# Performance work log

Hardware: AMD Instinct MI355X
Metric: run time of the kernel (lower is better)

The kernel has to match this reference:

```python
import jax, jax.numpy as jnp
import numpy as np

S, B = 64, 256
CH_IN, CH_OUT, AUX, HID = 128, 128, 3, 32
EPS = 1e-5


def _ln(h, g, b):
    mu = jnp.mean(h, axis=-1, keepdims=True)
    var = jnp.mean(jnp.square(h - mu), axis=-1, keepdims=True)
    return (h - mu) * jax.lax.rsqrt(var + EPS) * g + b


def _hyper_mlp(z, W1, b1, g1, be1, W2, b2, g2, be2, W3, b3):
    # Linear -> LN -> ReLU -> Linear -> LN -> ReLU -> Linear (droprate=0)
    h = jax.nn.relu(_ln(jnp.einsum('sba,ha->sbh', z, W1) + b1, g1, be1))
    h = jax.nn.relu(_ln(jnp.einsum('sbh,kh->sbk', h, W2) + b2, g2, be2))
    return jnp.einsum('sbh,oh->sbo', h, W3) + b3


def setup_inputs() -> dict:
    key = jax.random.key(0)
    ks = jax.random.split(key, 24)
    f = lambda k, shp: (jax.random.normal(k, shp, dtype=jnp.float32) * 0.05)
    inp = {
        'x': jax.random.normal(ks[0], (S, B, CH_IN), dtype=jnp.float32),
        'z': jax.random.normal(ks[1], (S, B, AUX), dtype=jnp.float32),
        # weight-branch hypernet params
        'wW1': f(ks[2], (HID, AUX)), 'wb1': jnp.zeros((HID,), jnp.float32),
        'wg1': jnp.ones((HID,), jnp.float32), 'wbe1': jnp.zeros((HID,), jnp.float32),
        'wW2': f(ks[3], (HID, HID)), 'wb2': jnp.zeros((HID,), jnp.float32),
        'wg2': jnp.ones((HID,), jnp.float32), 'wbe2': jnp.zeros((HID,), jnp.float32),
        'wW3': f(ks[4], (CH_OUT * CH_IN, HID)), 'wb3': jnp.zeros((CH_OUT * CH_IN,), jnp.float32),
        # bias-branch hypernet params
        'bW1': f(ks[5], (HID, AUX)), 'bb1': jnp.zeros((HID,), jnp.float32),
        'bg1': jnp.ones((HID,), jnp.float32), 'bbe1': jnp.zeros((HID,), jnp.float32),
        'bW2': f(ks[6], (HID, HID)), 'bb2': jnp.zeros((HID,), jnp.float32),
        'bg2': jnp.ones((HID,), jnp.float32), 'bbe2': jnp.zeros((HID,), jnp.float32),
        'bW3': f(ks[7], (CH_OUT, HID)), 'bb3': jnp.zeros((CH_OUT,), jnp.float32),
    }
    return inp


def reference(x, z,
              wW1, wb1, wg1, wbe1, wW2, wb2, wg2, wbe2, wW3, wb3,
              bW1, bb1, bg1, bbe1, bW2, bb2, bg2, bbe2, bW3, bb3):
    # per-token weight: [S,B,ch_out*ch_in] -> [S,B,ch_out,ch_in]
    weight = _hyper_mlp(z, wW1, wb1, wg1, wbe1, wW2, wb2, wg2, wbe2, wW3, wb3)
    weight = weight.reshape(S, B, CH_OUT, CH_IN)
    bias = _hyper_mlp(z, bW1, bb1, bg1, bbe1, bW2, bb2, bg2, bbe2, bW3, bb3)
    # batched mat-vec: out[s,b,o] = sum_i weight[s,b,o,i] * x[s,b,i] + bias
    out = jnp.einsum('sboi,sbi->sbo', weight, x) + bias
    return out
```

## Files before the change

### kernel.cpp

```cpp
#include <hip/hip_runtime.h>
#include <hip/hip_fp16.h>
#include <stdint.h>

#define KR      4288
#define LN_EPS  1e-5f

typedef _Float16 f16;
typedef __attribute__((ext_vector_type(2))) _Float16 h2v;
typedef __attribute__((ext_vector_type(4))) _Float16 h4v;
typedef __attribute__((ext_vector_type(8))) _Float16 h8v;
typedef __attribute__((ext_vector_type(4))) float    f32x4;

union H2U { uint32_t u; h2v h; };
union H8U { uint32_t u[4]; h8v v; };

__global__ __launch_bounds__(256) void prep_w3(
    const float* __restrict__ wW3, const float* __restrict__ wb3,
    const float* __restrict__ bW3, f16* __restrict__ w3h)
{
  const int cid = blockIdx.x * 256 + threadIdx.x;
  const int o   = blockIdx.y;
  if (cid >= KR / 8) return;
  const int k0    = cid * 8;
  const int slice = k0 >> 5;
  const int h0    = k0 & 31;
  float v[8];
  if (slice < 133) {
    const float* src;
    if      (slice < 128) src = wW3 + ((size_t)o * 128 + slice) * 32 + h0;
    else if (slice < 132) src = wb3 + (size_t)o * 128 + (slice - 128) * 32 + h0;
    else                  src = bW3 + (size_t)o * 32 + h0;
    float4 a = *(const float4*)src;
    float4 b = *(const float4*)(src + 4);
    v[0]=a.x; v[1]=a.y; v[2]=a.z; v[3]=a.w; v[4]=b.x; v[5]=b.y; v[6]=b.z; v[7]=b.w;
  } else {
#pragma unroll
    for (int j = 0; j < 8; ++j) v[j] = 0.f;
  }
  h8v pk;
#pragma unroll
  for (int j = 0; j < 8; ++j) pk[j] = (f16)v[j];
  *(h8v*)(w3h + (size_t)o * KR + k0) = pk;
}

__global__ __launch_bounds__(256) void fused_kernel(
    const float* __restrict__ x, const float* __restrict__ z,
    const float* __restrict__ wW1, const float* __restrict__ wb1,
    const float* __restrict__ wg1, const float* __restrict__ wbe1,
    const float* __restrict__ wW2, const float* __restrict__ wb2,
    const float* __restrict__ wg2, const float* __restrict__ wbe2,
    const float* __restrict__ bW1, const float* __restrict__ bb1,
    const float* __restrict__ bg1, const float* __restrict__ bbe1,
    const float* __restrict__ bW2, const float* __restrict__ bb2,
    const float* __restrict__ bg2, const float* __restrict__ bbe2,
    const float* __restrict__ bb3,
    const f16* __restrict__ w3h, float* __restrict__ out)
{
  __shared__ __align__(16) f16 xs[64][136];
  __shared__ __align__(16) f16 h2w_s[64][40];
  __shared__ __align__(16) f16 h2b_s[64][40];

  const int tid  = threadIdx.x;
  const int lane = tid & 63;
  const int wid  = tid >> 6;
  const int lm   = lane & 15, hc = lane >> 4, hbase = hc * 8;
  const int tile = blockIdx.x >> 1;
  const int kh   = blockIdx.x & 1;
  const int t0   = tile * 64;
  const int o0   = wid * 32;
  const int ks0    = kh * 34;
  const int n_iter = kh ? 33 : 34;

  float bbv[2];
#pragma unroll
  for (int n = 0; n < 2; ++n) bbv[n] = bb3[o0 + n * 16 + lm] * (float)kh;

  {
    const int r = tid >> 2, q = tid & 3;
    const float* src = x + (size_t)(t0 + r) * 128 + q * 32;
#pragma unroll
    for (int u = 0; u < 8; ++u) {
      float4 v = *(const float4*)(src + u * 4);
      h4v p; p[0] = (f16)v.x; p[1] = (f16)v.y; p[2] = (f16)v.z; p[3] = (f16)v.w;
      *(h4v*)&xs[r][q * 32 + u * 4] = p;
    }
  }

  if (tid < 128) {
    const int br  = tid >> 6;
    const int row = tid & 63;
    const int tok = t0 + row;
    const float* W1  = br ? bW1  : wW1;  const float* b1  = br ? bb1  : wb1;
    const float* g1  = br ? bg1  : wg1;  const float* be1 = br ? bbe1 : wbe1;
    const float* W2  = br ? bW2  : wW2;  const float* b2  = br ? bb2  : wb2;
    const float* g2  = br ? bg2  : wg2;  const float* be2 = br ? bbe2 : wbe2;

    const float z0 = z[tok * 3 + 0], z1 = z[tok * 3 + 1], z2 = z[tok * 3 + 2];

    float h1[32];
    float s = 0.f, s2 = 0.f;
#pragma unroll
    for (int j = 0; j < 32; ++j) {
      float v = W1[j * 3] * z0 + W1[j * 3 + 1] * z1 + W1[j * 3 + 2] * z2 + b1[j];
      h1[j] = v; s += v; s2 += v * v;
    }
    float mu  = s * (1.f / 32.f);
    float var = fmaxf(s2 * (1.f / 32.f) - mu * mu, 0.f);
    float rr  = rsqrtf(var + LN_EPS);
#pragma unroll
    for (int j = 0; j < 32; ++j)
      h1[j] = fmaxf((h1[j] - mu) * rr * g1[j] + be1[j], 0.f);

    float h2a[32];
    s = 0.f; s2 = 0.f;
#pragma unroll
    for (int j = 0; j < 32; ++j) {
      float acc = b2[j];
#pragma unroll
      for (int kk = 0; kk < 8; ++kk) {
        float4 w = *(const float4*)&W2[j * 32 + kk * 4];
        acc += w.x * h1[kk * 4] + w.y * h1[kk * 4 + 1]
             + w.z * h1[kk * 4 + 2] + w.w * h1[kk * 4 + 3];
      }
      h2a[j] = acc; s += acc; s2 += acc * acc;
    }
    mu  = s * (1.f / 32.f);
    var = fmaxf(s2 * (1.f / 32.f) - mu * mu, 0.f);
    rr  = rsqrtf(var + LN_EPS);
    f16* dst = br ? &h2b_s[row][0] : &h2w_s[row][0];
#pragma unroll
    for (int j4 = 0; j4 < 8; ++j4) {
      h4v w;
      w[0] = (f16)fmaxf((h2a[j4*4+0] - mu) * rr * g2[j4*4+0] + be2[j4*4+0], 0.f);
      w[1] = (f16)fmaxf((h2a[j4*4+1] - mu) * rr * g2[j4*4+1] + be2[j4*4+1], 0.f);
      w[2] = (f16)fmaxf((h2a[j4*4+2] - mu) * rr * g2[j4*4+2] + be2[j4*4+2], 0.f);
      w[3] = (f16)fmaxf((h2a[j4*4+3] - mu) * rr * g2[j4*4+3] + be2[j4*4+3], 0.f);
      *(h4v*)&dst[j4 * 4] = w;
    }
  }

  __syncthreads();

  uint32_t h2p[4][4];
#pragma unroll
  for (int m = 0; m < 4; ++m) {
    H8U c; c.v = *(const h8v*)&h2w_s[m * 16 + lm][hbase];
#pragma unroll
    for (int q = 0; q < 4; ++q) h2p[m][q] = c.u[q];
  }

  const f16* bp00 = w3h + (size_t)(o0 + lm)      * KR + (ks0 * 2    ) * 32 + hbase;
  const f16* bp01 = w3h + (size_t)(o0 + 16 + lm) * KR + (ks0 * 2    ) * 32 + hbase;
  const f16* bp10 = w3h + (size_t)(o0 + lm)      * KR + (ks0 * 2 + 1) * 32 + hbase;
  const f16* bp11 = w3h + (size_t)(o0 + 16 + lm) * KR + (ks0 * 2 + 1) * 32 + hbase;

#define LOADSET(S) do { \
    S[0][0] = *(const h8v*)bp00; bp00 += 64; \
    S[0][1] = *(const h8v*)bp01; bp01 += 64; \
    S[1][0] = *(const h8v*)bp10; bp10 += 64; \
    S[1][1] = *(const h8v*)bp11; bp11 += 64; } while (0)

  f32x4 acc[4][2];
#pragma unroll
  for (int m = 0; m < 4; ++m)
#pragma unroll
    for (int n = 0; n < 2; ++n) acc[m][n] = (f32x4){0.f, 0.f, 0.f, 0.f};

  auto STEP = [&](h8v (&bs)[2][2], int ks) {
    const int ksg = ks0 + ks;
    h8v af0[4], af1[4];
    if (ksg < 64) {
#pragma unroll
      for (int m = 0; m < 4; ++m) {
        const uint32_t xp = *(const uint32_t*)&xs[m * 16 + lm][2 * ksg];
        H2U x0, x1;
        x0.u = (xp & 0xffffu) | (xp << 16);
        x1.u = (xp >> 16) | (xp & 0xffff0000u);
        H8U r0, r1;
#pragma unroll
        for (int q = 0; q < 4; ++q) {
          H2U hq; hq.u = h2p[m][q];
          H2U p0; p0.h = x0.h * hq.h; r0.u[q] = p0.u;
          H2U p1; p1.h = x1.h * hq.h; r1.u[q] = p1.u;
        }
        af0[m] = r0.v; af1[m] = r1.v;
      }
    } else if (ksg < 66) {
      const int s = (ksg - 64) * 2;
#pragma unroll
      for (int m = 0; m < 4; ++m) {
        af0[m] = *(const h8v*)&xs[m * 16 + lm][s * 32 + hbase];
        af1[m] = *(const h8v*)&xs[m * 16 + lm][(s + 1) * 32 + hbase];
      }
    } else {
#pragma unroll
      for (int m = 0; m < 4; ++m) {
        af0[m] = *(const h8v*)&h2b_s[m * 16 + lm][hbase];
        af1[m] = af0[m];
      }
    }
#pragma unroll
    for (int n = 0; n < 2; ++n)
#pragma unroll
      for (int m = 0; m < 4; ++m)
        acc[m][n] = __builtin_amdgcn_mfma_f32_16x16x32_f16(af0[m], bs[0][n], acc[m][n], 0, 0, 0);
#pragma unroll
    for (int n = 0; n < 2; ++n)
#pragma unroll
      for (int m = 0; m < 4; ++m)
        acc[m][n] = __builtin_amdgcn_mfma_f32_16x16x32_f16(af1[m], bs[1][n], acc[m][n], 0, 0, 0);
  };

  h8v bA[2][2], bB[2][2];
  LOADSET(bA);
  LOADSET(bB);

  int ks = 0;
#pragma unroll 1
  while (ks + 2 <= n_iter) {
    STEP(bA, ks);
    if (ks + 2 < n_iter) LOADSET(bA);
    STEP(bB, ks + 1);
    if (ks + 3 < n_iter) LOADSET(bB);
    ks += 2;
  }
  if (ks < n_iter) STEP(bA, ks);

#pragma unroll
  for (int m = 0; m < 4; ++m) {
#pragma unroll
    for (int n = 0; n < 2; ++n) {
      const int gc = o0 + n * 16 + lm;
#pragma unroll
      for (int r_ = 0; r_ < 4; ++r_) {
        const int row = t0 + m * 16 + hc * 4 + r_;
        atomicAdd(&out[(size_t)row * 128 + gc], acc[m][n][r_] + bbv[n]);
      }
    }
  }
#undef LOADSET
}

extern "C" void kernel_launch(void* const* d_in, const int* in_sizes, int n_in,
                              void* d_out, int out_size, void* d_ws, size_t ws_size,
                              hipStream_t stream)
{
  const float* x    = (const float*)d_in[0];
  const float* z    = (const float*)d_in[1];
  const float* wW1  = (const float*)d_in[2];
  const float* wb1  = (const float*)d_in[3];
  const float* wg1  = (const float*)d_in[4];
  const float* wbe1 = (const float*)d_in[5];
  const float* wW2  = (const float*)d_in[6];
  const float* wb2  = (const float*)d_in[7];
  const float* wg2  = (const float*)d_in[8];
  const float* wbe2 = (const float*)d_in[9];
  const float* wW3  = (const float*)d_in[10];
  const float* wb3  = (const float*)d_in[11];
  const float* bW1  = (const float*)d_in[12];
  const float* bb1  = (const float*)d_in[13];
  const float* bg1  = (const float*)d_in[14];
  const float* bbe1 = (const float*)d_in[15];
  const float* bW2  = (const float*)d_in[16];
  const float* bb2  = (const float*)d_in[17];
  const float* bg2  = (const float*)d_in[18];
  const float* bbe2 = (const float*)d_in[19];
  const float* bW3  = (const float*)d_in[20];
  const float* bb3  = (const float*)d_in[21];

  f16*   w3h  = (f16*)d_ws;
  float* outf = (float*)d_out;

  hipMemsetAsync(d_out, 0, (size_t)16384 * 128 * sizeof(float), stream);
  hipLaunchKernelGGL(prep_w3, dim3(3, 128), dim3(256), 0, stream,
                     wW3, wb3, bW3, w3h);
  hipLaunchKernelGGL(fused_kernel, dim3(512), dim3(256), 0, stream,
                     x, z,
                     wW1, wb1, wg1, wbe1, wW2, wb2, wg2, wbe2,
                     bW1, bb1, bg1, bbe1, bW2, bb2, bg2, bbe2,
                     bb3, w3h, outf);
}
```

Before: 63.39 us.

## Split hypernet MLP into separate kernel and quad-split GEMM K dimension

```diff
diff --git a/kernel.cpp b/kernel.cpp
--- a/kernel.cpp
+++ b/kernel.cpp
@@ -2,7 +2,8 @@
 #include <hip/hip_fp16.h>
 #include <stdint.h>
 
-#define KR      4288
+#define T_DIM   16384
+#define NKS     67
 #define LN_EPS  1e-5f
 
 typedef _Float16 f16;
@@ -16,14 +17,21 @@
 
 __global__ __launch_bounds__(256) void prep_w3(
     const float* __restrict__ wW3, const float* __restrict__ wb3,
-    const float* __restrict__ bW3, f16* __restrict__ w3h)
+    const float* __restrict__ bW3, f16* __restrict__ w3p)
 {
-  const int cid = blockIdx.x * 256 + threadIdx.x;
-  const int o   = blockIdx.y;
-  if (cid >= KR / 8) return;
-  const int k0    = cid * 8;
-  const int slice = k0 >> 5;
-  const int h0    = k0 & 31;
+  const int idx  = blockIdx.x * 256 + threadIdx.x;
+  const int lane = idx & 63;
+  int rest = idx >> 6;
+  const int n  = rest & 1;  rest >>= 1;
+  const int i2 = rest & 1;  rest >>= 1;
+  const int ks = rest % 67;
+  const int os = rest / 67;
+  if (os >= 4) return;
+
+  const int o     = os * 32 + n * 16 + (lane & 15);
+  const int slice = ks * 2 + i2;
+  const int h0    = (lane >> 4) * 8;
+
   float v[8];
   if (slice < 133) {
     const float* src;
@@ -40,10 +48,10 @@
   h8v pk;
 #pragma unroll
   for (int j = 0; j < 8; ++j) pk[j] = (f16)v[j];
-  *(h8v*)(w3h + (size_t)o * KR + k0) = pk;
+  *(h8v*)(w3p + ((size_t)(os * 67 + ks) * 2048 + i2 * 1024 + n * 512 + lane * 8)) = pk;
 }
 
-__global__ __launch_bounds__(256) void fused_kernel(
+__global__ __launch_bounds__(256) void hyper_kernel(
     const float* __restrict__ x, const float* __restrict__ z,
     const float* __restrict__ wW1, const float* __restrict__ wb1,
     const float* __restrict__ wg1, const float* __restrict__ wbe1,
@@ -53,112 +61,128 @@
     const float* __restrict__ bg1, const float* __restrict__ bbe1,
     const float* __restrict__ bW2, const float* __restrict__ bb2,
     const float* __restrict__ bg2, const float* __restrict__ bbe2,
-    const float* __restrict__ bb3,
-    const f16* __restrict__ w3h, float* __restrict__ out)
+    f16* __restrict__ xf, f16* __restrict__ h2w, f16* __restrict__ h2b)
+{
+  const int tid = threadIdx.x;
+  const int bid = blockIdx.x;
+
+  {
+    const size_t base = (size_t)bid * 16384;
+#pragma unroll
+    for (int u = 0; u < 16; ++u) {
+      const size_t off = base + u * 1024 + tid * 4;
+      float4 a = *(const float4*)(x + off);
+      h4v p; p[0] = (f16)a.x; p[1] = (f16)a.y; p[2] = (f16)a.z; p[3] = (f16)a.w;
+      *(h4v*)(xf + off) = p;
+    }
+  }
+
+  const int br  = bid >> 6;
+  const int tok = (bid & 63) * 256 + tid;
+  const float* W1  = br ? bW1  : wW1;  const float* b1  = br ? bb1  : wb1;
+  const float* g1  = br ? bg1  : wg1;  const float* be1 = br ? bbe1 : wbe1;
+  const float* W2  = br ? bW2  : wW2;  const float* b2  = br ? bb2  : wb2;
+  const float* g2  = br ? bg2  : wg2;  const float* be2 = br ? bbe2 : wbe2;
+  f16* dst = (br ? h2b : h2w) + (size_t)tok * 32;
+
+  const float z0 = z[tok * 3 + 0], z1 = z[tok * 3 + 1], z2 = z[tok * 3 + 2];
+
+  float h1[32];
+  float s = 0.f, s2 = 0.f;
+#pragma unroll
+  for (int j = 0; j < 32; ++j) {
+    float v = W1[j * 3] * z0 + W1[j * 3 + 1] * z1 + W1[j * 3 + 2] * z2 + b1[j];
+    h1[j] = v; s += v; s2 += v * v;
+  }
+  float mu  = s * (1.f / 32.f);
+  float var = fmaxf(s2 * (1.f / 32.f) - mu * mu, 0.f);
+  float rr  = rsqrtf(var + LN_EPS);
+#pragma unroll
+  for (int j = 0; j < 32; ++j)
+    h1[j] = fmaxf((h1[j] - mu) * rr * g1[j] + be1[j], 0.f);
+
+  float h2a[32];
+  s = 0.f; s2 = 0.f;
+#pragma unroll
+  for (int j = 0; j < 32; ++j) {
+    float acc = b2[j];
+#pragma unroll
+    for (int kk = 0; kk < 8; ++kk) {
+      float4 w = *(const float4*)&W2[j * 32 + kk * 4];
+      acc += w.x * h1[kk * 4] + w.y * h1[kk * 4 + 1]
+           + w.z * h1[kk * 4 + 2] + w.w * h1[kk * 4 + 3];
+    }
+    h2a[j] = acc; s += acc; s2 += acc * acc;
+  }
+  mu  = s * (1.f / 32.f);
+  var = fmaxf(s2 * (1.f / 32.f) - mu * mu, 0.f);
+  rr  = rsqrtf(var + LN_EPS);
+#pragma unroll
+  for (int j8 = 0; j8 < 4; ++j8) {
+    h8v pk;
+#pragma unroll
+    for (int j = 0; j < 8; ++j)
+      pk[j] = (f16)fmaxf((h2a[j8*8+j] - mu) * rr * g2[j8*8+j] + be2[j8*8+j], 0.f);
+    *(h8v*)(dst + j8 * 8) = pk;
+  }
+}
+
+__global__ __launch_bounds__(256, 4) void gemm_kernel(
+    const f16* __restrict__ xf, const f16* __restrict__ w3p,
+    const f16* __restrict__ h2w, const f16* __restrict__ h2b,
+    const float* __restrict__ bb3, float* __restrict__ out)
 {
   __shared__ __align__(16) f16 xs[64][136];
-  __shared__ __align__(16) f16 h2w_s[64][40];
-  __shared__ __align__(16) f16 h2b_s[64][40];
 
   const int tid  = threadIdx.x;
   const int lane = tid & 63;
   const int wid  = tid >> 6;
   const int lm   = lane & 15, hc = lane >> 4, hbase = hc * 8;
-  const int tile = blockIdx.x >> 1;
-  const int kh   = blockIdx.x & 1;
+  const int tile = blockIdx.x >> 2;
+  const int q    = blockIdx.x & 3;
   const int t0   = tile * 64;
   const int o0   = wid * 32;
-  const int ks0    = kh * 34;
-  const int n_iter = kh ? 33 : 34;
+  const int ks0   = q * 17;
+  const int n_it  = (q == 3) ? 16 : 17;
+
+  {
+    const int r = tid >> 2, qq = tid & 3;
+    const f16* src = xf + (size_t)(t0 + r) * 128 + qq * 32;
+#pragma unroll
+    for (int u = 0; u < 4; ++u)
+      *(h8v*)&xs[r][qq * 32 + u * 8] = *(const h8v*)(src + u * 8);
+  }
+
+  uint32_t h2p[4][4];
+  short8_unused: ;
+  h8v h2bf[4];
+#pragma unroll
+  for (int m = 0; m < 4; ++m) {
+    H8U c; c.v = *(const h8v*)(h2w + (size_t)(t0 + m * 16 + lm) * 32 + hbase);
+#pragma unroll
+    for (int qq = 0; qq < 4; ++qq) h2p[m][qq] = c.u[qq];
+  }
+  if (q == 3) {
+#pragma unroll
+    for (int m = 0; m < 4; ++m)
+      h2bf[m] = *(const h8v*)(h2b + (size_t)(t0 + m * 16 + lm) * 32 + hbase);
+  }
 
   float bbv[2];
 #pragma unroll
-  for (int n = 0; n < 2; ++n) bbv[n] = bb3[o0 + n * 16 + lm] * (float)kh;
-
-  {
-    const int r = tid >> 2, q = tid & 3;
-    const float* src = x + (size_t)(t0 + r) * 128 + q * 32;
-#pragma unroll
-    for (int u = 0; u < 8; ++u) {
-      float4 v = *(const float4*)(src + u * 4);
-      h4v p; p[0] = (f16)v.x; p[1] = (f16)v.y; p[2] = (f16)v.z; p[3] = (f16)v.w;
-      *(h4v*)&xs[r][q * 32 + u * 4] = p;
-    }
-  }
-
-  if (tid < 128) {
-    const int br  = tid >> 6;
-    const int row = tid & 63;
-    const int tok = t0 + row;
-    const float* W1  = br ? bW1  : wW1;  const float* b1  = br ? bb1  : wb1;
-    const float* g1  = br ? bg1  : wg1;  const float* be1 = br ? bbe1 : wbe1;
-    const float* W2  = br ? bW2  : wW2;  const float* b2  = br ? bb2  : wb2;
-    const float* g2  = br ? bg2  : wg2;  const float* be2 = br ? bbe2 : wbe2;
-
-    const float z0 = z[tok * 3 + 0], z1 = z[tok * 3 + 1], z2 = z[tok * 3 + 2];
-
-    float h1[32];
-    float s = 0.f, s2 = 0.f;
-#pragma unroll
-    for (int j = 0; j < 32; ++j) {
-      float v = W1[j * 3] * z0 + W1[j * 3 + 1] * z1 + W1[j * 3 + 2] * z2 + b1[j];
-      h1[j] = v; s += v; s2 += v * v;
-    }
-    float mu  = s * (1.f / 32.f);
-    float var = fmaxf(s2 * (1.f / 32.f) - mu * mu, 0.f);
-    float rr  = rsqrtf(var + LN_EPS);
-#pragma unroll
-    for (int j = 0; j < 32; ++j)
-      h1[j] = fmaxf((h1[j] - mu) * rr * g1[j] + be1[j], 0.f);
-
-    float h2a[32];
-    s = 0.f; s2 = 0.f;
-#pragma unroll
-    for (int j = 0; j < 32; ++j) {
-      float acc = b2[j];
-#pragma unroll
-      for (int kk = 0; kk < 8; ++kk) {
-        float4 w = *(const float4*)&W2[j * 32 + kk * 4];
-        acc += w.x * h1[kk * 4] + w.y * h1[kk * 4 + 1]
-             + w.z * h1[kk * 4 + 2] + w.w * h1[kk * 4 + 3];
-      }
-      h2a[j] = acc; s += acc; s2 += acc * acc;
-    }
-    mu  = s * (1.f / 32.f);
-    var = fmaxf(s2 * (1.f / 32.f) - mu * mu, 0.f);
-    rr  = rsqrtf(var + LN_EPS);
-    f16* dst = br ? &h2b_s[row][0] : &h2w_s[row][0];
-#pragma unroll
-    for (int j4 = 0; j4 < 8; ++j4) {
-      h4v w;
-      w[0] = (f16)fmaxf((h2a[j4*4+0] - mu) * rr * g2[j4*4+0] + be2[j4*4+0], 0.f);
-      w[1] = (f16)fmaxf((h2a[j4*4+1] - mu) * rr * g2[j4*4+1] + be2[j4*4+1], 0.f);
-      w[2] = (f16)fmaxf((h2a[j4*4+2] - mu) * rr * g2[j4*4+2] + be2[j4*4+2], 0.f);
-      w[3] = (f16)fmaxf((h2a[j4*4+3] - mu) * rr * g2[j4*4+3] + be2[j4*4+3], 0.f);
-      *(h4v*)&dst[j4 * 4] = w;
-    }
-  }
+  for (int n = 0; n < 2; ++n)
+    bbv[n] = (q == 0) ? bb3[o0 + n * 16 + lm] : 0.f;
 
   __syncthreads();
 
-  uint32_t h2p[4][4];
-#pragma unroll
-  for (int m = 0; m < 4; ++m) {
-    H8U c; c.v = *(const h8v*)&h2w_s[m * 16 + lm][hbase];
-#pragma unroll
-    for (int q = 0; q < 4; ++q) h2p[m][q] = c.u[q];
-  }
-
-  const f16* bp00 = w3h + (size_t)(o0 + lm)      * KR + (ks0 * 2    ) * 32 + hbase;
-  const f16* bp01 = w3h + (size_t)(o0 + 16 + lm) * KR + (ks0 * 2    ) * 32 + hbase;
-  const f16* bp10 = w3h + (size_t)(o0 + lm)      * KR + (ks0 * 2 + 1) * 32 + hbase;
-  const f16* bp11 = w3h + (size_t)(o0 + 16 + lm) * KR + (ks0 * 2 + 1) * 32 + hbase;
+  const f16* bp = w3p + (size_t)(wid * 67 + ks0) * 2048 + lane * 8;
 
 #define LOADSET(S) do { \
-    S[0][0] = *(const h8v*)bp00; bp00 += 64; \
-    S[0][1] = *(const h8v*)bp01; bp01 += 64; \
-    S[1][0] = *(const h8v*)bp10; bp10 += 64; \
-    S[1][1] = *(const h8v*)bp11; bp11 += 64; } while (0)
+    S[0][0] = *(const h8v*)(bp); \
+    S[0][1] = *(const h8v*)(bp + 512); \
+    S[1][0] = *(const h8v*)(bp + 1024); \
+    S[1][1] = *(const h8v*)(bp + 1536); \
+    bp += 2048; } while (0)
 
   f32x4 acc[4][2];
 #pragma unroll
@@ -169,7 +193,7 @@
   auto STEP = [&](h8v (&bs)[2][2], int ks) {
     const int ksg = ks0 + ks;
     h8v af0[4], af1[4];
-    if (ksg < 64) {
+    if (__builtin_expect(ksg < 64, 1)) {
 #pragma unroll
       for (int m = 0; m < 4; ++m) {
         const uint32_t xp = *(const uint32_t*)&xs[m * 16 + lm][2 * ksg];
@@ -178,10 +202,10 @@
         x1.u = (xp >> 16) | (xp & 0xffff0000u);
         H8U r0, r1;
 #pragma unroll
-        for (int q = 0; q < 4; ++q) {
-          H2U hq; hq.u = h2p[m][q];
-          H2U p0; p0.h = x0.h * hq.h; r0.u[q] = p0.u;
-          H2U p1; p1.h = x1.h * hq.h; r1.u[q] = p1.u;
+        for (int qq = 0; qq < 4; ++qq) {
+          H2U hq; hq.u = h2p[m][qq];
+          H2U p0; p0.h = x0.h * hq.h; r0.u[qq] = p0.u;
+          H2U p1; p1.h = x1.h * hq.h; r1.u[qq] = p1.u;
         }
         af0[m] = r0.v; af1[m] = r1.v;
       }
@@ -194,10 +218,7 @@
       }
     } else {
 #pragma unroll
-      for (int m = 0; m < 4; ++m) {
-        af0[m] = *(const h8v*)&h2b_s[m * 16 + lm][hbase];
-        af1[m] = af0[m];
-      }
+      for (int m = 0; m < 4; ++m) { af0[m] = h2bf[m]; af1[m] = h2bf[m]; }
     }
 #pragma unroll
     for (int n = 0; n < 2; ++n)
@@ -217,14 +238,14 @@
 
   int ks = 0;
 #pragma unroll 1
-  while (ks + 2 <= n_iter) {
+  while (ks + 2 <= n_it) {
     STEP(bA, ks);
-    if (ks + 2 < n_iter) LOADSET(bA);
+    if (ks + 2 < n_it) LOADSET(bA);
     STEP(bB, ks + 1);
-    if (ks + 3 < n_iter) LOADSET(bB);
+    if (ks + 3 < n_it) LOADSET(bB);
     ks += 2;
   }
-  if (ks < n_iter) STEP(bA, ks);
+  if (ks < n_it) STEP(bA, ks);
 
 #pragma unroll
   for (int m = 0; m < 4; ++m) {
@@ -268,15 +289,20 @@
   const float* bW3  = (const float*)d_in[20];
   const float* bb3  = (const float*)d_in[21];
 
-  f16*   w3h  = (f16*)d_ws;
+  uint8_t* ws = (uint8_t*)d_ws;
+  f16* w3p = (f16*)ws;
+  f16* xf  = (f16*)(ws + 1097728);
+  f16* h2w = (f16*)(ws + 1097728 + 4194304);
+  f16* h2b = (f16*)(ws + 1097728 + 4194304 + 1048576);
   float* outf = (float*)d_out;
 
-  hipMemsetAsync(d_out, 0, (size_t)16384 * 128 * sizeof(float), stream);
-  hipLaunchKernelGGL(prep_w3, dim3(3, 128), dim3(256), 0, stream,
-                     wW3, wb3, bW3, w3h);
-  hipLaunchKernelGGL(fused_kernel, dim3(512), dim3(256), 0, stream,
+  hipMemsetAsync(d_out, 0, (size_t)T_DIM * 128 * sizeof(float), stream);
+  hipLaunchKernelGGL(prep_w3, dim3(268), dim3(256), 0, stream, wW3, wb3, bW3, w3p);
+  hipLaunchKernelGGL(hyper_kernel, dim3(128), dim3(256), 0, stream,
                      x, z,
                      wW1, wb1, wg1, wbe1, wW2, wb2, wg2, wbe2,
                      bW1, bb1, bg1, bbe1, bW2, bb2, bg2, bbe2,
-                     bb3, w3h, outf);
+                     xf, h2w, h2b);
+  hipLaunchKernelGGL(gemm_kernel, dim3(1024), dim3(256), 0, stream,
+                     xf, w3p, h2w, h2b, bb3, outf);
 }
```

After: 80.17 us. +26.5%, slower.
